# Optimization experiments

Hardware: AMD Instinct MI355X
Metric: run time of the kernel (lower is better)

The kernel has to match this reference:

```python
import jax, jax.numpy as jnp
import numpy as np

KERNEL_SIZE = 4
SCALE = 0.5


def setup_inputs() -> dict:
    key = jax.random.key(0)
    k1, k2, k3 = jax.random.split(key, 3)
    M, K, N = 16384, 1024, 4096
    x = jax.random.normal(k1, (M, K), dtype=jnp.float32)
    weight = jax.random.normal(k2, (N, K), dtype=jnp.float32)
    bias = jax.random.normal(k3, (N,), dtype=jnp.float32)
    return {"x": x, "weight": weight, "bias": bias}


def reference(x, weight, bias):
    # y = x @ W^T + b : (M, N)
    y = jnp.einsum('mk,nk->mn', x, weight) + bias[None, :]
    M, N = y.shape
    valid_n = (N // KERNEL_SIZE) * KERNEL_SIZE
    # MaxPool1d(kernel_size, stride=kernel_size): (M, N//k, k) -> max over window
    pooled = jnp.max(y[:, :valid_n].reshape(M, valid_n // KERNEL_SIZE, KERNEL_SIZE), axis=-1)
    # sum over pooled features, then scale -> (M,)
    return jnp.sum(pooled, axis=-1) * SCALE
```

## Files before the change

### kernel.cpp

```cpp
#include <hip/hip_runtime.h>
#include <stdint.h>

#define M_DIM 16384
#define K_DIM 1024
#define N_DIM 4096
#define BM 128
#define BN 128
#define LDSP 40

#define TILE_ELEMS (128 * K_DIM)
#define SLAB_ELEMS (128 * 32)
#define NSLAB_X ((M_DIM / 128) * 32)
#define NSLAB_W ((N_DIM / 128) * 32)
#define CROW 20

typedef __bf16 bf16;
typedef __attribute__((ext_vector_type(8))) __bf16 bf16x8;
typedef __attribute__((ext_vector_type(4))) float f32x4;

__device__ __forceinline__ uint32_t pack2_bf16(float a, float b) {
    uint32_t ua = __float_as_uint(a);
    uint32_t ub = __float_as_uint(b);
    ua += 0x7fffu + ((ua >> 16) & 1u);
    ub += 0x7fffu + ((ub >> 16) & 1u);
    return (ua >> 16) | (ub & 0xffff0000u);
}

__global__ __launch_bounds__(256) void convert_pack_kernel(
    const float* __restrict__ x, const float* __restrict__ w,
    bf16* __restrict__ xp, bf16* __restrict__ wp)
{
    int slab = blockIdx.x;
    const float* src;
    bf16* dst;
    if (slab < NSLAB_X) { src = x; dst = xp; }
    else                { slab -= NSLAB_X; src = w; dst = wp; }
    const int tile = slab >> 5;
    const int s    = slab & 31;

    __shared__ uint32_t ls[128 * CROW];

    const int t = threadIdx.x;
    {
        const int r  = t >> 1;
        const int kh = (t & 1) * 16;
        const float4* p = (const float4*)(src + (size_t)(tile * 128 + r) * K_DIM + s * 32 + kh);
        float4 a = p[0], b = p[1], c = p[2], d = p[3];
        uint4* lp = (uint4*)&ls[r * CROW + (t & 1) * 8];
        uint4 v0, v1;
        v0.x = pack2_bf16(a.x, a.y); v0.y = pack2_bf16(a.z, a.w);
        v0.z = pack2_bf16(b.x, b.y); v0.w = pack2_bf16(b.z, b.w);
        v1.x = pack2_bf16(c.x, c.y); v1.y = pack2_bf16(c.z, c.w);
        v1.z = pack2_bf16(d.x, d.y); v1.w = pack2_bf16(d.z, d.w);
        lp[0] = v0; lp[1] = v1;
    }
    __syncthreads();
    uint4* dst4 = (uint4*)(dst + (size_t)tile * TILE_ELEMS + (size_t)s * SLAB_ELEMS);
    #pragma unroll
    for (int p = 0; p < 2; ++p) {
        const int c    = t + p * 256;
        const int lane = c & 63;
        const int rb   = c >> 6;
        const int q    = lane >> 4;
        const int lrow = lane & 15;
        const int r    = rb * 16 + lrow;
        const uint4* lp = (const uint4*)&ls[r * CROW + q * 4];
        dst4[c] = lp[0];
    }
}

__device__ __forceinline__ void load_frags(const bf16* ga, const bf16* gb,
                                           bf16x8* af, bf16x8* bf) {
    #pragma unroll
    for (int i = 0; i < 4; ++i) af[i] = *(const bf16x8*)(ga + i * 512);
    #pragma unroll
    for (int j = 0; j < 4; ++j) bf[j] = *(const bf16x8*)(gb + j * 512);
}

__device__ __forceinline__ void do_mfma(const bf16x8* af, const bf16x8* bf,
                                        f32x4 acc[4][4]) {
    #pragma unroll
    for (int i = 0; i < 4; ++i)
        #pragma unroll
        for (int j = 0; j < 4; ++j)
            acc[i][j] = __builtin_amdgcn_mfma_f32_16x16x32_bf16(af[i], bf[j], acc[i][j], 0, 0, 0);
}

__global__ __launch_bounds__(256) void gemm_pool_direct_kernel(
    const bf16* __restrict__ xp, const bf16* __restrict__ wp,
    const float* __restrict__ bias, float* __restrict__ out)
{
    const int b  = blockIdx.x;
    const int by = (b & 7) * 16 + ((b >> 3) & 15);
    const int bx = b >> 7;

    const int lane = threadIdx.x & 63;
    const int wave = threadIdx.x >> 6;
    const int wm = wave >> 1;
    const int wn = wave & 1;
    const int lr = lane & 15;
    const int quad = lane >> 4;

    const bf16* Abase = xp + (size_t)by * TILE_ELEMS + (wm * 4) * 512 + lane * 8;
    const bf16* Bbase = wp + (size_t)bx * TILE_ELEMS + (wn * 4) * 512 + lane * 8;

    f32x4 acc[4][4] = {};
    bf16x8 aA[4], bA[4], aB[4], bB[4];

    load_frags(Abase, Bbase, aA, bA);
    #pragma unroll
    for (int s = 0; s < 32; s += 2) {
        load_frags(Abase + (s + 1) * SLAB_ELEMS, Bbase + (s + 1) * SLAB_ELEMS, aB, bB);
        do_mfma(aA, bA, acc);
        if (s + 2 < 32)
            load_frags(Abase + (s + 2) * SLAB_ELEMS, Bbase + (s + 2) * SLAB_ELEMS, aA, bA);
        do_mfma(aB, bB, acc);
    }

    float bv[4];
    #pragma unroll
    for (int j = 0; j < 4; ++j)
        bv[j] = bias[bx * BN + wn * 64 + j * 16 + lr];

    #pragma unroll
    for (int i = 0; i < 4; ++i) {
        float rs[4] = {0.f, 0.f, 0.f, 0.f};
        #pragma unroll
        for (int j = 0; j < 4; ++j) {
            #pragma unroll
            for (int r = 0; r < 4; ++r) {
                float t = acc[i][j][r] + bv[j];
                t = fmaxf(t, __shfl_xor(t, 1, 64));
                t = fmaxf(t, __shfl_xor(t, 2, 64));
                rs[r] += t;
            }
        }
        #pragma unroll
        for (int r = 0; r < 4; ++r) {
            rs[r] += __shfl_xor(rs[r], 4, 64);
            rs[r] += __shfl_xor(rs[r], 8, 64);
        }
        if (lr == 0) {
            const int row = by * BM + wm * 64 + i * 16 + quad * 4;
            #pragma unroll
            for (int r = 0; r < 4; ++r)
                atomicAdd(&out[row + r], rs[r] * 0.5f);
        }
    }
}

__global__ __launch_bounds__(256) void fused_linear_pool_kernel(
    const float* __restrict__ x, const float* __restrict__ wt,
    const float* __restrict__ bias, float* __restrict__ out)
{
    __shared__ uint32_t sA[BM * LDSP / 2];
    __shared__ uint32_t sB[BN * LDSP / 2];

    const int tid = threadIdx.x;
    const int bx = blockIdx.x;
    const int by = blockIdx.y;

    const float* Abase = x  + (size_t)by * BM * K_DIM;
    const float* Bbase = wt + (size_t)bx * BN * K_DIM;

    const int lane = tid & 63;
    const int wave = tid >> 6;
    const int wm = wave >> 1;
    const int wn = wave & 1;
    const int lr = lane & 15;
    const int quad = lane >> 4;

    const int srow  = tid >> 2;
    const int scol  = (tid & 3) * 8;
    const int swidx = (tid & 3) * 4;

    f32x4 acc[4][4] = {};

    for (int kt = 0; kt < K_DIM; kt += 32) {
        #pragma unroll
        for (int p = 0; p < 2; ++p) {
            const int r = srow + p * 64;
            const float4* ga = (const float4*)(Abase + (size_t)r * K_DIM + kt + scol);
            const float4* gb = (const float4*)(Bbase + (size_t)r * K_DIM + kt + scol);
            float4 a0 = ga[0], a1 = ga[1], b0 = gb[0], b1 = gb[1];
            uint4 wa;
            wa.x = pack2_bf16(a0.x, a0.y); wa.y = pack2_bf16(a0.z, a0.w);
            wa.z = pack2_bf16(a1.x, a1.y); wa.w = pack2_bf16(a1.z, a1.w);
            *(uint4*)&sA[r * (LDSP / 2) + swidx] = wa;
            uint4 wbv;
            wbv.x = pack2_bf16(b0.x, b0.y); wbv.y = pack2_bf16(b0.z, b0.w);
            wbv.z = pack2_bf16(b1.x, b1.y); wbv.w = pack2_bf16(b1.z, b1.w);
            *(uint4*)&sB[r * (LDSP / 2) + swidx] = wbv;
        }
        __syncthreads();

        bf16x8 af[4], bfr[4];
        #pragma unroll
        for (int i = 0; i < 4; ++i)
            af[i] = *(const bf16x8*)((const bf16*)sA + (wm * 64 + i * 16 + lr) * LDSP + quad * 8);
        #pragma unroll
        for (int j = 0; j < 4; ++j)
            bfr[j] = *(const bf16x8*)((const bf16*)sB + (wn * 64 + j * 16 + lr) * LDSP + quad * 8);

        #pragma unroll
        for (int i = 0; i < 4; ++i)
            #pragma unroll
            for (int j = 0; j < 4; ++j)
                acc[i][j] = __builtin_amdgcn_mfma_f32_16x16x32_bf16(af[i], bfr[j], acc[i][j], 0, 0, 0);
        __syncthreads();
    }

    float bv[4];
    #pragma unroll
    for (int j = 0; j < 4; ++j)
        bv[j] = bias[bx * BN + wn * 64 + j * 16 + lr];

    #pragma unroll
    for (int i = 0; i < 4; ++i) {
        float rsum[4] = {0.f, 0.f, 0.f, 0.f};
        #pragma unroll
        for (int j = 0; j < 4; ++j) {
            #pragma unroll
            for (int r = 0; r < 4; ++r) {
                float t = acc[i][j][r] + bv[j];
                t = fmaxf(t, __shfl_xor(t, 1, 64));
                t = fmaxf(t, __shfl_xor(t, 2, 64));
                t += __shfl_xor(t, 4, 64);
                t += __shfl_xor(t, 8, 64);
                rsum[r] += t;
            }
        }
        if (lr == 0) {
            const int row = by * BM + wm * 64 + i * 16 + quad * 4;
            #pragma unroll
            for (int r = 0; r < 4; ++r)
                atomicAdd(&out[row + r], rsum[r] * 0.5f);
        }
    }
}

extern "C" void kernel_launch(void* const* d_in, const int* in_sizes, int n_in,
                              void* d_out, int out_size, void* d_ws, size_t ws_size,
                              hipStream_t stream) {
    const float* x  = (const float*)d_in[0];
    const float* wt = (const float*)d_in[1];
    const float* bs = (const float*)d_in[2];
    float* out = (float*)d_out;

    hipMemsetAsync(out, 0, (size_t)out_size * sizeof(float), stream);

    const size_t xe = (size_t)M_DIM * K_DIM;
    const size_t we = (size_t)N_DIM * K_DIM;
    const size_t need = (xe + we) * sizeof(bf16);

    if (ws_size >= need) {
        bf16* xp = (bf16*)d_ws;
        bf16* wp = xp + xe;
        convert_pack_kernel<<<NSLAB_X + NSLAB_W, 256, 0, stream>>>(x, wt, xp, wp);
        gemm_pool_direct_kernel<<<(M_DIM / BM) * (N_DIM / BN), 256, 0, stream>>>(xp, wp, bs, out);
    } else {
        dim3 grid(N_DIM / BN, M_DIM / BM);
        fused_linear_pool_kernel<<<grid, 256, 0, stream>>>(x, wt, bs, out);
    }
}
```

Baseline: 270.7 us.

## Deepen B-fragment prefetch, remap block order per XCD, cap occupancy

Replaces the two-stage A/B register double-buffer with a three-deep prefetch ring for weight fragments and a two-deep ring for activation fragments, so global loads are issued further ahead of the MFMAs that consume them. It also changes the block-to-tile mapping so each XCD works on a contiguous 8-row group of M tiles across all N tiles in phases, aiming for better L2 reuse. Launch bounds now request three blocks per CU, which limits register use and can cause spills given the larger fragment buffers.

```diff
diff --git a/kernel.cpp b/kernel.cpp
--- a/kernel.cpp
+++ b/kernel.cpp
@@ -69,12 +69,9 @@
     }
 }
 
-__device__ __forceinline__ void load_frags(const bf16* ga, const bf16* gb,
-                                           bf16x8* af, bf16x8* bf) {
-    #pragma unroll
-    for (int i = 0; i < 4; ++i) af[i] = *(const bf16x8*)(ga + i * 512);
-    #pragma unroll
-    for (int j = 0; j < 4; ++j) bf[j] = *(const bf16x8*)(gb + j * 512);
+__device__ __forceinline__ void load_set(const bf16* g, bf16x8* f) {
+    #pragma unroll
+    for (int i = 0; i < 4; ++i) f[i] = *(const bf16x8*)(g + i * 512);
 }
 
 __device__ __forceinline__ void do_mfma(const bf16x8* af, const bf16x8* bf,
@@ -86,13 +83,16 @@
             acc[i][j] = __builtin_amdgcn_mfma_f32_16x16x32_bf16(af[i], bf[j], acc[i][j], 0, 0, 0);
 }
 
-__global__ __launch_bounds__(256) void gemm_pool_direct_kernel(
+__global__ __launch_bounds__(256, 3) void gemm_pool_direct_kernel(
     const bf16* __restrict__ xp, const bf16* __restrict__ wp,
     const float* __restrict__ bias, float* __restrict__ out)
 {
-    const int b  = blockIdx.x;
-    const int by = (b & 7) * 16 + ((b >> 3) & 15);
-    const int bx = b >> 7;
+    const int b     = blockIdx.x;
+    const int xcd   = b & 7;
+    const int o     = (b >> 3) & 7;
+    const int bx    = (b >> 6) & 31;
+    const int phase = b >> 11;
+    const int by    = phase * 64 + xcd * 8 + o;
 
     const int lane = threadIdx.x & 63;
     const int wave = threadIdx.x >> 6;
@@ -105,16 +105,18 @@
     const bf16* Bbase = wp + (size_t)bx * TILE_ELEMS + (wn * 4) * 512 + lane * 8;
 
     f32x4 acc[4][4] = {};
-    bf16x8 aA[4], bA[4], aB[4], bB[4];
-
-    load_frags(Abase, Bbase, aA, bA);
-    #pragma unroll
-    for (int s = 0; s < 32; s += 2) {
-        load_frags(Abase + (s + 1) * SLAB_ELEMS, Bbase + (s + 1) * SLAB_ELEMS, aB, bB);
-        do_mfma(aA, bA, acc);
-        if (s + 2 < 32)
-            load_frags(Abase + (s + 2) * SLAB_ELEMS, Bbase + (s + 2) * SLAB_ELEMS, aA, bA);
-        do_mfma(aB, bB, acc);
+    bf16x8 Af[2][4];
+    bf16x8 Bf[3][4];
+
+    load_set(Bbase, Bf[0]);
+    load_set(Bbase + SLAB_ELEMS, Bf[1]);
+    load_set(Abase, Af[0]);
+
+    #pragma unroll
+    for (int s = 0; s < 32; ++s) {
+        if (s + 2 < 32) load_set(Bbase + (s + 2) * SLAB_ELEMS, Bf[(s + 2) % 3]);
+        if (s + 1 < 32) load_set(Abase + (s + 1) * SLAB_ELEMS, Af[(s + 1) & 1]);
+        do_mfma(Af[s & 1], Bf[s % 3], acc);
     }
 
     float bv[4];
```

Result: no change. 268.5 us (-0.8%).
